# Kernel optimization log

Measured on AMD Instinct MI355X. Metric: run time of the kernel, lower is better.

Reference implementation:

```python
import jax, jax.numpy as jnp
import numpy as np

B, S, DM, H = 2, 4096, 512, 8
DEPTH = DM // H


def setup_inputs() -> dict:
    key = jax.random.key(0)
    ks = jax.random.split(key, 12)
    scale = 1.0 / np.sqrt(DM)
    return {
        "q": jax.random.normal(ks[0], (B, S, DM), jnp.float32),
        "k": jax.random.normal(ks[1], (B, S, DM), jnp.float32),
        "v": jax.random.normal(ks[2], (B, S, DM), jnp.float32),
        # padding-style mask: 1.0 = masked position, 0.0 = attend
        "mask": jax.random.bernoulli(ks[3], 0.1, (B, 1, 1, S)).astype(jnp.float32),
        "Wq": jax.random.normal(ks[4], (DM, DM), jnp.float32) * scale,
        "bq": jnp.zeros((DM,), jnp.float32),
        "Wk": jax.random.normal(ks[5], (DM, DM), jnp.float32) * scale,
        "bk": jnp.zeros((DM,), jnp.float32),
        "Wv": jax.random.normal(ks[6], (DM, DM), jnp.float32) * scale,
        "bv": jnp.zeros((DM,), jnp.float32),
        "Wo": jax.random.normal(ks[7], (DM, DM), jnp.float32) * scale,
        "bo": jnp.zeros((DM,), jnp.float32),
    }


def _split_heads(x):
    # [B, S, DM] -> [B, H, S, DEPTH]
    b, s, _ = x.shape
    return x.reshape(b, s, H, DEPTH).transpose(0, 2, 1, 3)


def reference(q, k, v, mask, Wq, bq, Wk, bk, Wv, bv, Wo, bo):
    qh = _split_heads(q @ Wq + bq)   # [B,H,S,D]
    kh = _split_heads(k @ Wk + bk)
    vh = _split_heads(v @ Wv + bv)
    logits = jnp.einsum("bhqd,bhkd->bhqk", qh, kh) / jnp.sqrt(
        jnp.asarray(DEPTH, qh.dtype))
    logits = logits + mask * (-1e9)
    attn = jax.nn.softmax(logits, axis=-1)          # [B,H,Sq,Sk]
    out = jnp.einsum("bhqk,bhkd->bhqd", attn, vh)   # [B,H,S,D]
    out = out.transpose(0, 2, 1, 3).reshape(q.shape[0], -1, DM)
    return out @ Wo + bo
```

## Files before the change

### kernel.cpp

```cpp
#include <hip/hip_runtime.h>
#include <math.h>

#define BDIM 2
#define SDIM 4096
#define DMODEL 512
#define NHEAD 8
#define DHEAD 64
#define MROWS (BDIM * SDIM)

typedef __attribute__((ext_vector_type(8))) short short8;
typedef __attribute__((ext_vector_type(4))) float f32x4;

#define MFMA16(a, b, c) __builtin_amdgcn_mfma_f32_16x16x32_bf16((a), (b), (c), 0, 0, 0)
#define EXP2F(x) __builtin_amdgcn_exp2f(x)

#define SCALE2 0.18033688011112042f
#define MASKMUL -1.442695040e9f
#define M0C 16.0f

#define GLOAD_LDS16(g, l)                                                     \
  __builtin_amdgcn_global_load_lds(                                           \
      (const __attribute__((address_space(1))) void*)(g),                     \
      (__attribute__((address_space(3))) void*)(l), 16, 0, 0)

__device__ inline void bf16_split(float x, short& h, short& l) {
  unsigned u = __float_as_uint(x);
  h = (short)(u >> 16);
  float hf = __uint_as_float(u & 0xffff0000u);
  l = (short)(__float_as_uint(x - hf) >> 16);
}

__global__ __launch_bounds__(256) void wsplit_kernel(
    const float* __restrict__ W0, const float* __restrict__ W1,
    const float* __restrict__ W2, const float* __restrict__ W3,
    short* __restrict__ T0h, short* __restrict__ T0l, short* __restrict__ T1h,
    short* __restrict__ T1l, short* __restrict__ T2h, short* __restrict__ T2l,
    short* __restrict__ T3h, short* __restrict__ T3l) {
  __shared__ short Th[64 * 72], Tl[64 * 72];
  const int tid = threadIdx.x;
  const int k0 = blockIdx.x * 64;
  const int n0 = blockIdx.y * 64;
  const int z = blockIdx.z;
  const float* W = (z == 0) ? W0 : (z == 1) ? W1 : (z == 2) ? W2 : W3;
  short* Oh = (z == 0) ? T0h : (z == 1) ? T1h : (z == 2) ? T2h : T3h;
  short* Ol = (z == 0) ? T0l : (z == 1) ? T1l : (z == 2) ? T2l : T3l;

  {
    const int r = tid >> 2;
    const int c16 = (tid & 3) * 16;
    short8 h0, h1, l0, l1;
#pragma unroll
    for (int g = 0; g < 2; g++) {
      const f32x4 a = *(const f32x4*)(W + (size_t)(k0 + r) * DMODEL + n0 + c16 + g * 8);
      const f32x4 b = *(const f32x4*)(W + (size_t)(k0 + r) * DMODEL + n0 + c16 + g * 8 + 4);
      short8& hh = g ? h1 : h0;
      short8& ll = g ? l1 : l0;
#pragma unroll
      for (int j = 0; j < 4; j++) {
        short x, y;
        bf16_split(a[j], x, y);
        hh[j] = x;
        ll[j] = y;
        bf16_split(b[j], x, y);
        hh[4 + j] = x;
        ll[4 + j] = y;
      }
    }
    *(short8*)&Th[r * 72 + c16] = h0;
    *(short8*)&Th[r * 72 + c16 + 8] = h1;
    *(short8*)&Tl[r * 72 + c16] = l0;
    *(short8*)&Tl[r * 72 + c16 + 8] = l1;
  }
  __syncthreads();
  {
    const int n = tid >> 2;
    const int kc = (tid & 3) * 16;
    short8 h0, h1, l0, l1;
#pragma unroll
    for (int i = 0; i < 8; i++) {
      h0[i] = Th[(kc + i) * 72 + n];
      h1[i] = Th[(kc + 8 + i) * 72 + n];
      l0[i] = Tl[(kc + i) * 72 + n];
      l1[i] = Tl[(kc + 8 + i) * 72 + n];
    }
    short* dh = Oh + (size_t)(n0 + n) * DMODEL + k0 + kc;
    short* dl = Ol + (size_t)(n0 + n) * DMODEL + k0 + kc;
    *(short8*)dh = h0;
    *(short8*)(dh + 8) = h1;
    *(short8*)dl = l0;
    *(short8*)(dl + 8) = l1;
  }
}

template <int MODE>
__global__ __launch_bounds__(512, 2) void proj3_kernel(
    const float* __restrict__ X, const short* __restrict__ Wth,
    const short* __restrict__ Wtl, const float* __restrict__ bias,
    float* __restrict__ out, short* __restrict__ oh, short* __restrict__ ol) {
  __shared__ short L[2 * 20480];
  const int tid = threadIdx.x;
  const int lane = tid & 63;
  const int w = tid >> 6;
  const int lane15 = lane & 15;
  const int quad = lane >> 4;
  const int m0 = blockIdx.x * 64;
  const int n0 = blockIdx.y * 256;
  const int wm = (w >> 2) * 32;
  const int wn = (w & 3) * 64;

  const char* gp[5];
  int stepb[5], ldso[5];
#pragma unroll
  for (int i = 0; i < 5; i++) {
    const int idx = w * 5 + i;
    if (idx < 8) {
      const int g = idx * 64 + lane;
      gp[i] = (const char*)(X + (size_t)(m0 + (g >> 3)) * DMODEL + (g & 7) * 4);
      stepb[i] = 128;
    } else {
      const int gg = idx * 64 + lane - 512;
      const short* src = (gg < 1024) ? Wth : Wtl;
      const int a = gg & 1023;
      gp[i] = (const char*)(src + (size_t)(n0 + (a >> 2)) * DMODEL + (a & 3) * 8);
      stepb[i] = 64;
    }
    ldso[i] = idx * 512;
  }

  f32x4 c[2][4];
#pragma unroll
  for (int mt = 0; mt < 2; mt++)
#pragma unroll
    for (int nt = 0; nt < 4; nt++) c[mt][nt] = (f32x4){0.f, 0.f, 0.f, 0.f};

  constexpr int NT = DMODEL / 32;

#pragma unroll
  for (int i = 0; i < 5; i++) GLOAD_LDS16(gp[i], &L[ldso[i]]);

  for (int t = 0; t < NT; t++) {
    __syncthreads();
    if (t + 1 < NT) {
      short* dst = &L[((t + 1) & 1) * 20480];
#pragma unroll
      for (int i = 0; i < 5; i++)
        GLOAD_LDS16(gp[i] + (t + 1) * stepb[i], dst + ldso[i]);
    }
    const short* buf = &L[(t & 1) * 20480];
    const float* Af = (const float*)buf;
    short8 ah[2], al[2], bh[4], bl[4];
#pragma unroll
    for (int mt = 0; mt < 2; mt++) {
      const int r = wm + mt * 16 + lane15;
      const f32x4 a0 = *(const f32x4*)&Af[r * 32 + quad * 8];
      const f32x4 a1 = *(const f32x4*)&Af[r * 32 + quad * 8 + 4];
#pragma unroll
      for (int j = 0; j < 4; j++) {
        short x, y;
        bf16_split(a0[j], x, y);
        ah[mt][j] = x;
        al[mt][j] = y;
        bf16_split(a1[j], x, y);
        ah[mt][4 + j] = x;
        al[mt][4 + j] = y;
      }
    }
#pragma unroll
    for (int nt = 0; nt < 4; nt++) {
      const int r = wn + nt * 16 + lane15;
      bh[nt] = *(const short8*)&buf[4096 + r * 32 + quad * 8];
      bl[nt] = *(const short8*)&buf[12288 + r * 32 + quad * 8];
    }
    __builtin_amdgcn_s_setprio(1);
#pragma unroll
    for (int mt = 0; mt < 2; mt++)
#pragma unroll
      for (int nt = 0; nt < 4; nt++) {
        c[mt][nt] = MFMA16(ah[mt], bh[nt], c[mt][nt]);
        c[mt][nt] = MFMA16(ah[mt], bl[nt], c[mt][nt]);
        c[mt][nt] = MFMA16(al[mt], bh[nt], c[mt][nt]);
      }
    __builtin_amdgcn_s_setprio(0);
  }

#pragma unroll
  for (int nt = 0; nt < 4; nt++) {
    const int n = n0 + wn + nt * 16 + lane15;
    const float bb = bias[n];
#pragma unroll
    for (int mt = 0; mt < 2; mt++)
#pragma unroll
      for (int r = 0; r < 4; r++) {
        const int m = m0 + wm + mt * 16 + quad * 4 + r;
        const float val = c[mt][nt][r] + bb;
        if (MODE == 1) {
          const int bidx = m >> 12;
          const int s = m & 4095;
          const int hh = n >> 6;
          const int d = n & 63;
          const size_t off =
              ((size_t)(bidx * NHEAD + hh) * SDIM + s) * DHEAD + d;
          short x, y;
          bf16_split(val, x, y);
          oh[off] = x;
          ol[off] = y;
        } else {
          out[(size_t)m * DMODEL + n] = val;
        }
      }
  }
}

__global__ __launch_bounds__(256) void vtrans_kernel(
    const short* __restrict__ vh, const short* __restrict__ vl,
    short* __restrict__ vth, short* __restrict__ vtl) {
  __shared__ short Th[64 * 72], Tl[64 * 72];
  const int tid = threadIdx.x;
  const int s0 = blockIdx.x * 64;
  const int h = blockIdx.y;
  const int b = blockIdx.z;
  const size_t base = (size_t)(b * NHEAD + h) * SDIM * DHEAD;

  {
    const int s = tid >> 2;
    const int c = tid & 3;
    const short* srcH = vh + base + (size_t)(s0 + s) * DHEAD + c * 16;
    const short* srcL = vl + base + (size_t)(s0 + s) * DHEAD + c * 16;
    *(short8*)&Th[s * 72 + c * 16] = *(const short8*)srcH;
    *(short8*)&Th[s * 72 + c * 16 + 8] = *(const short8*)(srcH + 8);
    *(short8*)&Tl[s * 72 + c * 16] = *(const short8*)srcL;
    *(short8*)&Tl[s * 72 + c * 16 + 8] = *(const short8*)(srcL + 8);
  }
  __syncthreads();
  {
    const int d = tid & 63;
    const int cw = tid >> 6;
    short8 a0, a1, b0, b1;
#pragma unroll
    for (int i = 0; i < 8; i++) {
      a0[i] = Th[(cw * 16 + i) * 72 + d];
      a1[i] = Th[(cw * 16 + 8 + i) * 72 + d];
      b0[i] = Tl[(cw * 16 + i) * 72 + d];
      b1[i] = Tl[(cw * 16 + 8 + i) * 72 + d];
    }
    short* dstH = vth + base + (size_t)d * SDIM + s0 + cw * 16;
    short* dstL = vtl + base + (size_t)d * SDIM + s0 + cw * 16;
    *(short8*)dstH = a0;
    *(short8*)(dstH + 8) = a1;
    *(short8*)dstL = b0;
    *(short8*)(dstL + 8) = b1;
  }
}

#define KP 72
#define VP 72
#define PP 68

__global__ __launch_bounds__(256, 1) void flash_attn_kernel(
    const short* __restrict__ qhh, const short* __restrict__ qhl,
    const short* __restrict__ khh, const short* __restrict__ khl,
    const short* __restrict__ vth, const short* __restrict__ vtl,
    const float* __restrict__ mask, float* __restrict__ ctx) {
  __shared__ short Ksh[64 * KP], Ksl[64 * KP];
  __shared__ short Vsh[64 * VP], Vsl[64 * VP];
  __shared__ float Ps[256 * PP];

  const int tid = threadIdx.x;
  const int lane = tid & 63;
  const int w = tid >> 6;
  const int lane15 = lane & 15;
  const int quad = lane >> 4;

  const int bid = blockIdx.x + 16 * (blockIdx.y + NHEAD * blockIdx.z);
  const int sw = (bid & 7) * 32 + (bid >> 3);
  const int q0 = (sw & 15) * 256;
  const int h = (sw >> 4) & 7;
  const int b = sw >> 7;

  const size_t base = (size_t)(b * NHEAD + h) * SDIM * DHEAD;
  const short* Qh = qhh + base;
  const short* Ql = qhl + base;
  const short* Kh = khh + base;
  const short* Kl = khl + base;
  const short* Vh = vth + base;
  const short* Vl = vtl + base;
  const float* mb = mask + (size_t)b * SDIM;

  short8 qfh[4][2], qfl[4][2];
#pragma unroll
  for (int mt = 0; mt < 4; mt++) {
    const size_t row = q0 + w * 64 + mt * 16 + lane15;
#pragma unroll
    for (int ks = 0; ks < 2; ks++) {
      qfh[mt][ks] = *(const short8*)(Qh + row * DHEAD + ks * 32 + quad * 8);
      qfl[mt][ks] = *(const short8*)(Ql + row * DHEAD + ks * 32 + quad * 8);
    }
  }

  f32x4 o[4][4];
#pragma unroll
  for (int mt = 0; mt < 4; mt++)
#pragma unroll
    for (int dt = 0; dt < 4; dt++) o[mt][dt] = (f32x4){0.f, 0.f, 0.f, 0.f};
  float lr[4][4];
#pragma unroll
  for (int mt = 0; mt < 4; mt++)
#pragma unroll
    for (int r = 0; r < 4; r++) lr[mt][r] = 0.f;

  short8 onesb;
#pragma unroll
  for (int j = 0; j < 8; j++) onesb[j] = (short)0x3F80;

  const int sr = tid >> 2;
  const int sc = (tid & 3) * 16;

  short8 rg[8];
  rg[0] = *(const short8*)(Kh + (size_t)sr * DHEAD + sc);
  rg[1] = *(const short8*)(Kh + (size_t)sr * DHEAD + sc + 8);
  rg[2] = *(const short8*)(Kl + (size_t)sr * DHEAD + sc);
  rg[3] = *(const short8*)(Kl + (size_t)sr * DHEAD + sc + 8);
  rg[4] = *(const short8*)(Vh + (size_t)sr * SDIM + sc);
  rg[5] = *(const short8*)(Vh + (size_t)sr * SDIM + sc + 8);
  rg[6] = *(const short8*)(Vl + (size_t)sr * SDIM + sc);
  rg[7] = *(const short8*)(Vl + (size_t)sr * SDIM + sc + 8);

  for (int kt = 0; kt < SDIM / 64; kt++) {
    const int k0 = kt * 64;
    __builtin_amdgcn_s_barrier();
    __builtin_amdgcn_sched_barrier(0);
    *(short8*)&Ksh[sr * KP + sc] = rg[0];
    *(short8*)&Ksh[sr * KP + sc + 8] = rg[1];
    *(short8*)&Ksl[sr * KP + sc] = rg[2];
    *(short8*)&Ksl[sr * KP + sc + 8] = rg[3];
    *(short8*)&Vsh[sr * VP + sc] = rg[4];
    *(short8*)&Vsh[sr * VP + sc + 8] = rg[5];
    *(short8*)&Vsl[sr * VP + sc] = rg[6];
    *(short8*)&Vsl[sr * VP + sc + 8] = rg[7];
    if (kt + 1 < SDIM / 64) {
      const int k1 = k0 + 64;
      rg[0] = *(const short8*)(Kh + (size_t)(k1 + sr) * DHEAD + sc);
      rg[1] = *(const short8*)(Kh + (size_t)(k1 + sr) * DHEAD + sc + 8);
      rg[2] = *(const short8*)(Kl + (size_t)(k1 + sr) * DHEAD + sc);
      rg[3] = *(const short8*)(Kl + (size_t)(k1 + sr) * DHEAD + sc + 8);
      rg[4] = *(const short8*)(Vh + (size_t)sr * SDIM + k1 + sc);
      rg[5] = *(const short8*)(Vh + (size_t)sr * SDIM + k1 + sc + 8);
      rg[6] = *(const short8*)(Vl + (size_t)sr * SDIM + k1 + sc);
      rg[7] = *(const short8*)(Vl + (size_t)sr * SDIM + k1 + sc + 8);
    }
    float mv[4];
#pragma unroll
    for (int nt = 0; nt < 4; nt++)
      mv[nt] = fmaf(mb[k0 + nt * 16 + lane15], MASKMUL, -M0C);
    asm volatile("s_waitcnt lgkmcnt(0)" ::: "memory");
    __builtin_amdgcn_s_barrier();
    __builtin_amdgcn_sched_barrier(0);

    __builtin_amdgcn_s_setprio(1);
#pragma unroll
    for (int nt = 0; nt < 4; nt++) {
      short8 kbh[2], kbl[2];
#pragma unroll
      for (int ks = 0; ks < 2; ks++) {
        const int koff = (nt * 16 + lane15) * KP + ks * 32 + quad * 8;
        kbh[ks] = *(const short8*)&Ksh[koff];
        kbl[ks] = *(const short8*)&Ksl[koff];
      }
#pragma unroll
      for (int mt = 0; mt < 4; mt++) {
        f32x4 acc = (f32x4){0.f, 0.f, 0.f, 0.f};
#pragma unroll
        for (int ks = 0; ks < 2; ks++) {
          acc = MFMA16(qfh[mt][ks], kbh[ks], acc);
          acc = MFMA16(qfh[mt][ks], kbl[ks], acc);
          acc = MFMA16(qfl[mt][ks], kbh[ks], acc);
        }
#pragma unroll
        for (int r = 0; r < 4; r++) {
          const float p = EXP2F(fmaf(acc[r], SCALE2, mv[nt]));
          Ps[(w * 64 + mt * 16 + quad * 4 + r) * PP + nt * 16 + lane15] = p;
        }
      }
    }
    __builtin_amdgcn_s_setprio(0);

    short8 pah[4][2], pal[4][2];
#pragma unroll
    for (int mt = 0; mt < 4; mt++)
#pragma unroll
      for (int kf = 0; kf < 2; kf++) {
        const float* pr =
            &Ps[(w * 64 + mt * 16 + lane15) * PP + kf * 32 + quad * 8];
        const f32x4 p0 = *(const f32x4*)pr;
        const f32x4 p1 = *(const f32x4*)(pr + 4);
        short8 ph, pl;
#pragma unroll
        for (int j = 0; j < 4; j++) {
          short hh, ll;
          bf16_split(p0[j], hh, ll);
          ph[j] = hh;
          pl[j] = ll;
        }
#pragma unroll
        for (int j = 0; j < 4; j++) {
          short hh, ll;
          bf16_split(p1[j], hh, ll);
          ph[4 + j] = hh;
          pl[4 + j] = ll;
        }
        pah[mt][kf] = ph;
        pal[mt][kf] = pl;
      }

    __builtin_amdgcn_s_setprio(1);
#pragma unroll
    for (int mt = 0; mt < 4; mt++) {
      f32x4 racc = (f32x4){0.f, 0.f, 0.f, 0.f};
#pragma unroll
      for (int kf = 0; kf < 2; kf++) {
        racc = MFMA16(pah[mt][kf], onesb, racc);
        racc = MFMA16(pal[mt][kf], onesb, racc);
      }
#pragma unroll
      for (int r = 0; r < 4; r++) lr[mt][r] += racc[r];
    }

#pragma unroll
    for (int dt = 0; dt < 4; dt++)
#pragma unroll
      for (int kf = 0; kf < 2; kf++) {
        const int voff = (dt * 16 + lane15) * VP + kf * 32 + quad * 8;
        const short8 vbh = *(const short8*)&Vsh[voff];
        const short8 vbl = *(const short8*)&Vsl[voff];
#pragma unroll
        for (int mt = 0; mt < 4; mt++) {
          o[mt][dt] = MFMA16(pah[mt][kf], vbh, o[mt][dt]);
          o[mt][dt] = MFMA16(pah[mt][kf], vbl, o[mt][dt]);
          o[mt][dt] = MFMA16(pal[mt][kf], vbh, o[mt][dt]);
        }
      }
    __builtin_amdgcn_s_setprio(0);
  }

  float inv[4][4];
#pragma unroll
  for (int mt = 0; mt < 4; mt++)
#pragma unroll
    for (int r = 0; r < 4; r++) inv[mt][r] = 1.f / lr[mt][r];
#pragma unroll
  for (int mt = 0; mt < 4; mt++)
#pragma unroll
    for (int dt = 0; dt < 4; dt++)
#pragma unroll
      for (int r = 0; r < 4; r++) {
        const int q = q0 + w * 64 + mt * 16 + quad * 4 + r;
        const int col = h * DHEAD + dt * 16 + lane15;
        ctx[((size_t)b * SDIM + q) * DMODEL + col] = o[mt][dt][r] * inv[mt][r];
      }
}

extern "C" void kernel_launch(void* const* d_in, const int* in_sizes, int n_in,
                              void* d_out, int out_size, void* d_ws,
                              size_t ws_size, hipStream_t stream) {
  const float* q = (const float*)d_in[0];
  const float* k = (const float*)d_in[1];
  const float* v = (const float*)d_in[2];
  const float* mask = (const float*)d_in[3];
  const float* Wq = (const float*)d_in[4];
  const float* bq = (const float*)d_in[5];
  const float* Wk = (const float*)d_in[6];
  const float* bk = (const float*)d_in[7];
  const float* Wv = (const float*)d_in[8];
  const float* bv = (const float*)d_in[9];
  const float* Wo = (const float*)d_in[10];
  const float* bo = (const float*)d_in[11];
  float* out = (float*)d_out;

  char* W = (char*)d_ws;
  const size_t SZB = (size_t)MROWS * DMODEL * sizeof(short);
  short* q_h = (short*)(W + 0 * SZB);
  short* q_l = (short*)(W + 1 * SZB);
  short* k_h = (short*)(W + 2 * SZB);
  short* k_l = (short*)(W + 3 * SZB);
  short* v_h = (short*)(W + 4 * SZB);
  short* v_l = (short*)(W + 5 * SZB);
  short* vt_h = (short*)(W + 6 * SZB);
  short* vt_l = (short*)(W + 7 * SZB);
  float* ctx = (float*)(W + 4 * SZB);
  const size_t WSZ = (size_t)DMODEL * DMODEL * sizeof(short);
  char* WT = W + 8 * SZB;
  short* wtq_h = (short*)(WT + 0 * WSZ);
  short* wtq_l = (short*)(WT + 1 * WSZ);
  short* wtk_h = (short*)(WT + 2 * WSZ);
  short* wtk_l = (short*)(WT + 3 * WSZ);
  short* wtv_h = (short*)(WT + 4 * WSZ);
  short* wtv_l = (short*)(WT + 5 * WSZ);
  short* wto_h = (short*)(WT + 6 * WSZ);
  short* wto_l = (short*)(WT + 7 * WSZ);

  wsplit_kernel<<<dim3(DMODEL / 64, DMODEL / 64, 4), 256, 0, stream>>>(
      Wq, Wk, Wv, Wo, wtq_h, wtq_l, wtk_h, wtk_l, wtv_h, wtv_l, wto_h, wto_l);

  const dim3 gp2(MROWS / 64, DMODEL / 256);

  proj3_kernel<1><<<gp2, 512, 0, stream>>>(q, wtq_h, wtq_l, bq, nullptr, q_h,
                                           q_l);
  proj3_kernel<1><<<gp2, 512, 0, stream>>>(k, wtk_h, wtk_l, bk, nullptr, k_h,
                                           k_l);
  proj3_kernel<1><<<gp2, 512, 0, stream>>>(v, wtv_h, wtv_l, bv, nullptr, v_h,
                                           v_l);

  vtrans_kernel<<<dim3(SDIM / 64, NHEAD, BDIM), 256, 0, stream>>>(v_h, v_l,
                                                                  vt_h, vt_l);

  flash_attn_kernel<<<dim3(SDIM / 256, NHEAD, BDIM), 256, 0, stream>>>(
      q_h, q_l, k_h, k_l, vt_h, vt_l, mask, ctx);

  proj3_kernel<0><<<gp2, 512, 0, stream>>>(ctx, wto_h, wto_l, bo, out, nullptr,
                                           nullptr);
}
```

Baseline: 446.8 us.

## Batch QKV projections, fuse V transpose, shrink flash tile to 128 rows

The three Q/K/V projection launches become one batched launch over blockIdx.z. The V projection writes its transposed layout directly through an LDS staging pass, which removes the separate transpose kernel and its intermediate buffers. The flash-attention block tile drops from 256 to 128 query rows, with 2 blocks per CU and a smaller LDS P buffer, to raise occupancy and block count. bf16 hi/lo splitting now packs pairs with perm instructions. The smaller tile halves K/V reuse per block, and the runtime mode branch adds some generality cost.

```diff
diff --git a/kernel.cpp b/kernel.cpp
--- a/kernel.cpp
+++ b/kernel.cpp
@@ -10,6 +10,12 @@
 
 typedef __attribute__((ext_vector_type(8))) short short8;
 typedef __attribute__((ext_vector_type(4))) float f32x4;
+typedef __attribute__((ext_vector_type(4))) int i32x4;
+
+union S8I4 {
+  short8 s;
+  i32x4 i;
+};
 
 #define MFMA16(a, b, c) __builtin_amdgcn_mfma_f32_16x16x32_bf16((a), (b), (c), 0, 0, 0)
 #define EXP2F(x) __builtin_amdgcn_exp2f(x)
@@ -28,6 +34,17 @@
   h = (short)(u >> 16);
   float hf = __uint_as_float(u & 0xffff0000u);
   l = (short)(__float_as_uint(x - hf) >> 16);
+}
+
+__device__ inline int2 bf16_split_pack(float x0, float x1) {
+  const unsigned u0 = __float_as_uint(x0), u1 = __float_as_uint(x1);
+  const float d0 = x0 - __uint_as_float(u0 & 0xffff0000u);
+  const float d1 = x1 - __uint_as_float(u1 & 0xffff0000u);
+  int2 r;
+  r.x = __builtin_amdgcn_perm(u1, u0, 0x07060302);
+  r.y = __builtin_amdgcn_perm(__float_as_uint(d1), __float_as_uint(d0),
+                              0x07060302);
+  return r;
 }
 
 __global__ __launch_bounds__(256) void wsplit_kernel(
@@ -92,11 +109,16 @@
   }
 }
 
-template <int MODE>
-__global__ __launch_bounds__(512, 2) void proj3_kernel(
-    const float* __restrict__ X, const short* __restrict__ Wth,
-    const short* __restrict__ Wtl, const float* __restrict__ bias,
-    float* __restrict__ out, short* __restrict__ oh, short* __restrict__ ol) {
+__global__ __launch_bounds__(512, 2) void proj4_kernel(
+    const int mode_sel, const float* __restrict__ X0,
+    const float* __restrict__ X1, const float* __restrict__ X2,
+    const short* __restrict__ Wth0, const short* __restrict__ Wth1,
+    const short* __restrict__ Wth2, const short* __restrict__ Wtl0,
+    const short* __restrict__ Wtl1, const short* __restrict__ Wtl2,
+    const float* __restrict__ bias0, const float* __restrict__ bias1,
+    const float* __restrict__ bias2, float* __restrict__ out,
+    short* __restrict__ qoh, short* __restrict__ qol, short* __restrict__ koh,
+    short* __restrict__ kol, short* __restrict__ vth, short* __restrict__ vtl) {
   __shared__ short L[2 * 20480];
   const int tid = threadIdx.x;
   const int lane = tid & 63;
@@ -105,6 +127,14 @@
   const int quad = lane >> 4;
   const int m0 = blockIdx.x * 64;
   const int n0 = blockIdx.y * 256;
+  const int z = blockIdx.z;
+  const int mode = (mode_sel >= 0) ? mode_sel : (z == 2 ? 2 : 1);
+  const float* X = (z == 0) ? X0 : (z == 1) ? X1 : X2;
+  const short* Wth = (z == 0) ? Wth0 : (z == 1) ? Wth1 : Wth2;
+  const short* Wtl = (z == 0) ? Wtl0 : (z == 1) ? Wtl1 : Wtl2;
+  const float* bias = (z == 0) ? bias0 : (z == 1) ? bias1 : bias2;
+  short* oh = (z == 0) ? qoh : koh;
+  short* ol = (z == 0) ? qol : kol;
   const int wm = (w >> 2) * 32;
   const int wn = (w & 3) * 64;
 
@@ -154,16 +184,17 @@
       const int r = wm + mt * 16 + lane15;
       const f32x4 a0 = *(const f32x4*)&Af[r * 32 + quad * 8];
       const f32x4 a1 = *(const f32x4*)&Af[r * 32 + quad * 8 + 4];
-#pragma unroll
-      for (int j = 0; j < 4; j++) {
-        short x, y;
-        bf16_split(a0[j], x, y);
-        ah[mt][j] = x;
-        al[mt][j] = y;
-        bf16_split(a1[j], x, y);
-        ah[mt][4 + j] = x;
-        al[mt][4 + j] = y;
-      }
+      S8I4 hh, ll;
+      const int2 p0 = bf16_split_pack(a0[0], a0[1]);
+      const int2 p1 = bf16_split_pack(a0[2], a0[3]);
+      const int2 p2 = bf16_split_pack(a1[0], a1[1]);
+      const int2 p3 = bf16_split_pack(a1[2], a1[3]);
+      hh.i[0] = p0.x; ll.i[0] = p0.y;
+      hh.i[1] = p1.x; ll.i[1] = p1.y;
+      hh.i[2] = p2.x; ll.i[2] = p2.y;
+      hh.i[3] = p3.x; ll.i[3] = p3.y;
+      ah[mt] = hh.s;
+      al[mt] = ll.s;
     }
 #pragma unroll
     for (int nt = 0; nt < 4; nt++) {
@@ -183,6 +214,41 @@
     __builtin_amdgcn_s_setprio(0);
   }
 
+  if (mode == 2) {
+    __syncthreads();
+    short* Lh = L;
+    short* Ll = L + 18432;
+#pragma unroll
+    for (int nt = 0; nt < 4; nt++) {
+      const int n = wn + nt * 16 + lane15;
+      const float bb = bias[n0 + n];
+#pragma unroll
+      for (int mt = 0; mt < 2; mt++)
+#pragma unroll
+        for (int r = 0; r < 4; r++) {
+          const int m = wm + mt * 16 + quad * 4 + r;
+          short x, y;
+          bf16_split(c[mt][nt][r] + bb, x, y);
+          Lh[n * 72 + m] = x;
+          Ll[n * 72 + m] = y;
+        }
+    }
+    __syncthreads();
+    const int row = tid >> 1;
+    const int half = tid & 1;
+    const int n = n0 + row;
+    const int hh = n >> 6, d = n & 63;
+    const int bidx = m0 >> 12, s0 = m0 & 4095;
+    const size_t tbase = ((size_t)(bidx * NHEAD + hh)) * SDIM * DHEAD +
+                         (size_t)d * SDIM + s0 + half * 32;
+#pragma unroll
+    for (int i = 0; i < 4; i++) {
+      *(short8*)(vth + tbase + i * 8) = *(const short8*)&Lh[row * 72 + half * 32 + i * 8];
+      *(short8*)(vtl + tbase + i * 8) = *(const short8*)&Ll[row * 72 + half * 32 + i * 8];
+    }
+    return;
+  }
+
 #pragma unroll
   for (int nt = 0; nt < 4; nt++) {
     const int n = n0 + wn + nt * 16 + lane15;
@@ -193,7 +259,7 @@
       for (int r = 0; r < 4; r++) {
         const int m = m0 + wm + mt * 16 + quad * 4 + r;
         const float val = c[mt][nt][r] + bb;
-        if (MODE == 1) {
+        if (mode == 1) {
           const int bidx = m >> 12;
           const int s = m & 4095;
           const int hh = n >> 6;
@@ -211,59 +277,18 @@
   }
 }
 
-__global__ __launch_bounds__(256) void vtrans_kernel(
-    const short* __restrict__ vh, const short* __restrict__ vl,
-    short* __restrict__ vth, short* __restrict__ vtl) {
-  __shared__ short Th[64 * 72], Tl[64 * 72];
-  const int tid = threadIdx.x;
-  const int s0 = blockIdx.x * 64;
-  const int h = blockIdx.y;
-  const int b = blockIdx.z;
-  const size_t base = (size_t)(b * NHEAD + h) * SDIM * DHEAD;
-
-  {
-    const int s = tid >> 2;
-    const int c = tid & 3;
-    const short* srcH = vh + base + (size_t)(s0 + s) * DHEAD + c * 16;
-    const short* srcL = vl + base + (size_t)(s0 + s) * DHEAD + c * 16;
-    *(short8*)&Th[s * 72 + c * 16] = *(const short8*)srcH;
-    *(short8*)&Th[s * 72 + c * 16 + 8] = *(const short8*)(srcH + 8);
-    *(short8*)&Tl[s * 72 + c * 16] = *(const short8*)srcL;
-    *(short8*)&Tl[s * 72 + c * 16 + 8] = *(const short8*)(srcL + 8);
-  }
-  __syncthreads();
-  {
-    const int d = tid & 63;
-    const int cw = tid >> 6;
-    short8 a0, a1, b0, b1;
-#pragma unroll
-    for (int i = 0; i < 8; i++) {
-      a0[i] = Th[(cw * 16 + i) * 72 + d];
-      a1[i] = Th[(cw * 16 + 8 + i) * 72 + d];
-      b0[i] = Tl[(cw * 16 + i) * 72 + d];
-      b1[i] = Tl[(cw * 16 + 8 + i) * 72 + d];
-    }
-    short* dstH = vth + base + (size_t)d * SDIM + s0 + cw * 16;
-    short* dstL = vtl + base + (size_t)d * SDIM + s0 + cw * 16;
-    *(short8*)dstH = a0;
-    *(short8*)(dstH + 8) = a1;
-    *(short8*)dstL = b0;
-    *(short8*)(dstL + 8) = b1;
-  }
-}
-
 #define KP 72
 #define VP 72
 #define PP 68
 
-__global__ __launch_bounds__(256, 1) void flash_attn_kernel(
+__global__ __launch_bounds__(256, 2) void flash_attn_kernel(
     const short* __restrict__ qhh, const short* __restrict__ qhl,
     const short* __restrict__ khh, const short* __restrict__ khl,
     const short* __restrict__ vth, const short* __restrict__ vtl,
     const float* __restrict__ mask, float* __restrict__ ctx) {
   __shared__ short Ksh[64 * KP], Ksl[64 * KP];
   __shared__ short Vsh[64 * VP], Vsl[64 * VP];
-  __shared__ float Ps[256 * PP];
+  __shared__ float Ps[128 * PP];
 
   const int tid = threadIdx.x;
   const int lane = tid & 63;
@@ -271,11 +296,11 @@
   const int lane15 = lane & 15;
   const int quad = lane >> 4;
 
-  const int bid = blockIdx.x + 16 * (blockIdx.y + NHEAD * blockIdx.z);
-  const int sw = (bid & 7) * 32 + (bid >> 3);
-  const int q0 = (sw & 15) * 256;
-  const int h = (sw >> 4) & 7;
-  const int b = sw >> 7;
+  const int bid = blockIdx.x + 32 * (blockIdx.y + NHEAD * blockIdx.z);
+  const int sw = (bid & 7) * 64 + (bid >> 3);
+  const int q0 = (sw & 31) * 128;
+  const int h = (sw >> 5) & 7;
+  const int b = sw >> 8;
 
   const size_t base = (size_t)(b * NHEAD + h) * SDIM * DHEAD;
   const short* Qh = qhh + base;
@@ -286,10 +311,10 @@
   const short* Vl = vtl + base;
   const float* mb = mask + (size_t)b * SDIM;
 
-  short8 qfh[4][2], qfl[4][2];
-#pragma unroll
-  for (int mt = 0; mt < 4; mt++) {
-    const size_t row = q0 + w * 64 + mt * 16 + lane15;
+  short8 qfh[2][2], qfl[2][2];
+#pragma unroll
+  for (int mt = 0; mt < 2; mt++) {
+    const size_t row = q0 + w * 32 + mt * 16 + lane15;
 #pragma unroll
     for (int ks = 0; ks < 2; ks++) {
       qfh[mt][ks] = *(const short8*)(Qh + row * DHEAD + ks * 32 + quad * 8);
@@ -297,14 +322,14 @@
     }
   }
 
-  f32x4 o[4][4];
-#pragma unroll
-  for (int mt = 0; mt < 4; mt++)
+  f32x4 o[2][4];
+#pragma unroll
+  for (int mt = 0; mt < 2; mt++)
 #pragma unroll
     for (int dt = 0; dt < 4; dt++) o[mt][dt] = (f32x4){0.f, 0.f, 0.f, 0.f};
-  float lr[4][4];
-#pragma unroll
-  for (int mt = 0; mt < 4; mt++)
+  float lr[2][4];
+#pragma unroll
+  for (int mt = 0; mt < 2; mt++)
 #pragma unroll
     for (int r = 0; r < 4; r++) lr[mt][r] = 0.f;
 
@@ -367,7 +392,7 @@
         kbl[ks] = *(const short8*)&Ksl[koff];
       }
 #pragma unroll
-      for (int mt = 0; mt < 4; mt++) {
+      for (int mt = 0; mt < 2; mt++) {
         f32x4 acc = (f32x4){0.f, 0.f, 0.f, 0.f};
 #pragma unroll
         for (int ks = 0; ks < 2; ks++) {
@@ -378,43 +403,37 @@
 #pragma unroll
         for (int r = 0; r < 4; r++) {
           const float p = EXP2F(fmaf(acc[r], SCALE2, mv[nt]));
-          Ps[(w * 64 + mt * 16 + quad * 4 + r) * PP + nt * 16 + lane15] = p;
+          Ps[(w * 32 + mt * 16 + quad * 4 + r) * PP + nt * 16 + lane15] = p;
         }
       }
     }
     __builtin_amdgcn_s_setprio(0);
 
-    short8 pah[4][2], pal[4][2];
-#pragma unroll
-    for (int mt = 0; mt < 4; mt++)
+    short8 pah[2][2], pal[2][2];
+#pragma unroll
+    for (int mt = 0; mt < 2; mt++)
 #pragma unroll
       for (int kf = 0; kf < 2; kf++) {
         const float* pr =
-            &Ps[(w * 64 + mt * 16 + lane15) * PP + kf * 32 + quad * 8];
+            &Ps[(w * 32 + mt * 16 + lane15) * PP + kf * 32 + quad * 8];
         const f32x4 p0 = *(const f32x4*)pr;
         const f32x4 p1 = *(const f32x4*)(pr + 4);
-        short8 ph, pl;
-#pragma unroll
-        for (int j = 0; j < 4; j++) {
-          short hh, ll;
-          bf16_split(p0[j], hh, ll);
-          ph[j] = hh;
-          pl[j] = ll;
-        }
-#pragma unroll
-        for (int j = 0; j < 4; j++) {
-          short hh, ll;
-          bf16_split(p1[j], hh, ll);
-          ph[4 + j] = hh;
-          pl[4 + j] = ll;
-        }
-        pah[mt][kf] = ph;
-        pal[mt][kf] = pl;
+        S8I4 ph, pl;
+        const int2 r0 = bf16_split_pack(p0[0], p0[1]);
+        const int2 r1 = bf16_split_pack(p0[2], p0[3]);
+        const int2 r2 = bf16_split_pack(p1[0], p1[1]);
+        const int2 r3 = bf16_split_pack(p1[2], p1[3]);
+        ph.i[0] = r0.x; pl.i[0] = r0.y;
+        ph.i[1] = r1.x; pl.i[1] = r1.y;
+        ph.i[2] = r2.x; pl.i[2] = r2.y;
+        ph.i[3] = r3.x; pl.i[3] = r3.y;
+        pah[mt][kf] = ph.s;
+        pal[mt][kf] = pl.s;
       }
 
     __builtin_amdgcn_s_setprio(1);
 #pragma unroll
-    for (int mt = 0; mt < 4; mt++) {
+    for (int mt = 0; mt < 2; mt++) {
       f32x4 racc = (f32x4){0.f, 0.f, 0.f, 0.f};
 #pragma unroll
       for (int kf = 0; kf < 2; kf++) {
@@ -433,7 +452,7 @@
         const short8 vbh = *(const short8*)&Vsh[voff];
         const short8 vbl = *(const short8*)&Vsl[voff];
 #pragma unroll
-        for (int mt = 0; mt < 4; mt++) {
+        for (int mt = 0; mt < 2; mt++) {
           o[mt][dt] = MFMA16(pah[mt][kf], vbh, o[mt][dt]);
           o[mt][dt] = MFMA16(pah[mt][kf], vbl, o[mt][dt]);
           o[mt][dt] = MFMA16(pal[mt][kf], vbh, o[mt][dt]);
@@ -442,18 +461,18 @@
     __builtin_amdgcn_s_setprio(0);
   }
 
-  float inv[4][4];
-#pragma unroll
-  for (int mt = 0; mt < 4; mt++)
+  float inv[2][4];
+#pragma unroll
+  for (int mt = 0; mt < 2; mt++)
 #pragma unroll
     for (int r = 0; r < 4; r++) inv[mt][r] = 1.f / lr[mt][r];
 #pragma unroll
-  for (int mt = 0; mt < 4; mt++)
+  for (int mt = 0; mt < 2; mt++)
 #pragma unroll
     for (int dt = 0; dt < 4; dt++)
 #pragma unroll
       for (int r = 0; r < 4; r++) {
-        const int q = q0 + w * 64 + mt * 16 + quad * 4 + r;
+        const int q = q0 + w * 32 + mt * 16 + quad * 4 + r;
         const int col = h * DHEAD + dt * 16 + lane15;
         ctx[((size_t)b * SDIM + q) * DMODEL + col] = o[mt][dt][r] * inv[mt][r];
       }
@@ -482,11 +501,9 @@
   short* q_l = (short*)(W + 1 * SZB);
   short* k_h = (short*)(W + 2 * SZB);
   short* k_l = (short*)(W + 3 * SZB);
-  short* v_h = (short*)(W + 4 * SZB);
-  short* v_l = (short*)(W + 5 * SZB);
-  short* vt_h = (short*)(W + 6 * SZB);
-  short* vt_l = (short*)(W + 7 * SZB);
-  float* ctx = (float*)(W + 4 * SZB);
+  short* vt_h = (short*)(W + 4 * SZB);
+  short* vt_l = (short*)(W + 5 * SZB);
+  float* ctx = (float*)(W + 6 * SZB);
   const size_t WSZ = (size_t)DMODEL * DMODEL * sizeof(short);
   char* WT = W + 8 * SZB;
   short* wtq_h = (short*)(WT + 0 * WSZ);
@@ -501,21 +518,15 @@
   wsplit_kernel<<<dim3(DMODEL / 64, DMODEL / 64, 4), 256, 0, stream>>>(
       Wq, Wk, Wv, Wo, wtq_h, wtq_l, wtk_h, wtk_l, wtv_h, wtv_l, wto_h, wto_l);
 
-  const dim3 gp2(MROWS / 64, DMODEL / 256);
-
-  proj3_kernel<1><<<gp2, 512, 0, stream>>>(q, wtq_h, wtq_l, bq, nullptr, q_h,
-                                           q_l);
-  proj3_kernel<1><<<gp2, 512, 0, stream>>>(k, wtk_h, wtk_l, bk, nullptr, k_h,
-                                           k_l);
-  proj3_kernel<1><<<gp2, 512, 0, stream>>>(v, wtv_h, wtv_l, bv, nullptr, v_h,
-                                           v_l);
-
-  vtrans_kernel<<<dim3(SDIM / 64, NHEAD, BDIM), 256, 0, stream>>>(v_h, v_l,
-                                                                  vt_h, vt_l);
-
-  flash_attn_kernel<<<dim3(SDIM / 256, NHEAD, BDIM), 256, 0, stream>>>(
+  proj4_kernel<<<dim3(MROWS / 64, DMODEL / 256, 3), 512, 0, stream>>>(
+      -1, q, k, v, wtq_h, wtk_h, wtv_h, wtq_l, wtk_l, wtv_l, bq, bk, bv,
+      nullptr, q_h, q_l, k_h, k_l, vt_h, vt_l);
+
+  flash_attn_kernel<<<dim3(SDIM / 128, NHEAD, BDIM), 256, 0, stream>>>(
       q_h, q_l, k_h, k_l, vt_h, vt_l, mask, ctx);
 
-  proj3_kernel<0><<<gp2, 512, 0, stream>>>(ctx, wto_h, wto_l, bo, out, nullptr,
-                                           nullptr);
+  proj4_kernel<<<dim3(MROWS / 64, DMODEL / 256, 1), 512, 0, stream>>>(
+      0, ctx, nullptr, nullptr, wto_h, nullptr, nullptr, wto_l, nullptr,
+      nullptr, bo, nullptr, nullptr, out, nullptr, nullptr, nullptr, nullptr,
+      nullptr, nullptr);
 }
```

Result: faster. 368.9 us (-17.4%).
